# Kernel tuning notes

Hardware: AMD Instinct MI355X
Metric: run time of the kernel (lower is better)

Reference implementation:

```python
import jax, jax.numpy as jnp
import numpy as np

B, N, IN_DIM, HID, OUT_DIM = 8, 1024, 768, 128, 768
H1, H2, MHA_HEADS, C = 8, 1, 4, 32
ALPHA = 0.2
NEG = -9e15
LN_EPS = 1e-5


def _gat_layer(x, W, a1, a2, adj_mask):
    # x: [B,N,Fin], W: [H,Fin,Fout], a1/a2: [H,Fout], adj_mask: [B,N,N] bool
    h = jnp.einsum('bni,hio->bhno', x, W)                      # [B,H,N,F]
    s1 = jnp.einsum('bhno,ho->bhn', h, a1)                     # score for source node i
    s2 = jnp.einsum('bhno,ho->bhn', h, a2)                     # score for target node j
    e = jax.nn.leaky_relu(s1[:, :, :, None] + s2[:, :, None, :], negative_slope=ALPHA)
    e = jnp.where(adj_mask[:, None, :, :], e, NEG)
    attn = jax.nn.softmax(e, axis=-1)                          # [B,H,N,N]
    hp = jnp.einsum('bhnm,bhmo->bhno', attn, h)                # [B,H,N,F]
    b, nh, n, f = hp.shape
    return hp.transpose(0, 2, 1, 3).reshape(b, n, nh * f)      # concat heads -> [B,N,H*F]


def _mha(q, k, v, wq, bq, wk, bk, wv, bv, wo, bo, n_heads):
    # torch-style MultiheadAttention (eval, no dropout). q:[B,Lq,E] k,v:[B,Lk,E]
    b, lq, e = q.shape
    lk = k.shape[1]
    hd = e // n_heads
    Q = (q @ wq + bq).reshape(b, lq, n_heads, hd).transpose(0, 2, 1, 3)
    K = (k @ wk + bk).reshape(b, lk, n_heads, hd).transpose(0, 2, 1, 3)
    V = (v @ wv + bv).reshape(b, lk, n_heads, hd).transpose(0, 2, 1, 3)
    scores = jnp.einsum('bhqd,bhkd->bhqk', Q, K) / jnp.sqrt(jnp.float32(hd))
    attn = jax.nn.softmax(scores, axis=-1)
    out = jnp.einsum('bhqk,bhkd->bhqd', attn, V)
    out = out.transpose(0, 2, 1, 3).reshape(b, lq, e)
    return out @ wo + bo


def _layernorm(x, g, b):
    mu = jnp.mean(x, axis=-1, keepdims=True)
    var = jnp.var(x, axis=-1, keepdims=True)
    return (x - mu) * jax.lax.rsqrt(var + LN_EPS) * g + b


def setup_inputs() -> dict:
    key = jax.random.key(0)
    ks = jax.random.split(key, 24)
    s = lambda fan_in: 1.0 / np.sqrt(fan_in)
    inp = {
        'node_features': jax.random.normal(ks[0], (B, N, IN_DIM), jnp.float32),
        'adjacency': jax.random.randint(ks[1], (B, N, N), 0, 2, jnp.int32),
        'context_indices': jax.random.randint(ks[2], (B, C), 0, N, jnp.int32),
        # GAT layer 1: 8 heads, in=768 -> out=128 each
        'W1': jax.random.normal(ks[3], (H1, IN_DIM, HID), jnp.float32) * s(IN_DIM),
        'a1_1': jax.random.normal(ks[4], (H1, HID), jnp.float32) * s(2 * HID),
        'a2_1': jax.random.normal(ks[5], (H1, HID), jnp.float32) * s(2 * HID),
        # GAT layer 2: 1 head, in=1024 -> out=128
        'W2': jax.random.normal(ks[6], (H2, HID * H1, HID), jnp.float32) * s(HID * H1),
        'a1_2': jax.random.normal(ks[7], (H2, HID), jnp.float32) * s(2 * HID),
        'a2_2': jax.random.normal(ks[8], (H2, HID), jnp.float32) * s(2 * HID),
        # query MultiheadAttention (embed_dim=128, 4 heads)
        'wq': jax.random.normal(ks[9], (HID, HID), jnp.float32) * s(HID),
        'bq': jnp.zeros((HID,), jnp.float32),
        'wk': jax.random.normal(ks[10], (HID, HID), jnp.float32) * s(HID),
        'bk': jnp.zeros((HID,), jnp.float32),
        'wv': jax.random.normal(ks[11], (HID, HID), jnp.float32) * s(HID),
        'bv': jnp.zeros((HID,), jnp.float32),
        'wo': jax.random.normal(ks[12], (HID, HID), jnp.float32) * s(HID),
        'bo': jnp.zeros((HID,), jnp.float32),
        # projection MLP
        'p1_w': jax.random.normal(ks[13], (HID, HID), jnp.float32) * s(HID),
        'p1_b': jnp.zeros((HID,), jnp.float32),
        'ln_g': jnp.ones((HID,), jnp.float32),
        'ln_b': jnp.zeros((HID,), jnp.float32),
        'p2_w': jax.random.normal(ks[14], (HID, OUT_DIM), jnp.float32) * s(HID),
        'p2_b': jnp.zeros((OUT_DIM,), jnp.float32),
    }
    return inp


def reference(node_features, adjacency, context_indices,
              W1, a1_1, a2_1, W2, a1_2, a2_2,
              wq, bq, wk, bk, wv, bv, wo, bo,
              p1_w, p1_b, ln_g, ln_b, p2_w, p2_b):
    adj_mask = adjacency > 0
    h = jax.nn.elu(_gat_layer(node_features, W1, a1_1, a2_1, adj_mask))  # [B,N,1024]
    h = jax.nn.elu(_gat_layer(h, W2, a1_2, a2_2, adj_mask))              # [B,N,128]
    q = h[:, 0:1, :]                                                      # [B,1,E]
    ctx = jnp.take_along_axis(h, context_indices[:, :, None], axis=1)     # [B,C,E]
    pooled = _mha(q, ctx, ctx, wq, bq, wk, bk, wv, bv, wo, bo, MHA_HEADS)[:, 0, :]
    z = jax.nn.relu(_layernorm(pooled @ p1_w + p1_b, ln_g, ln_b))
    return z @ p2_w + p2_b                                                # [B,OUT_DIM]
```

## Files before the change

### kernel.cpp

```cpp
#include <hip/hip_runtime.h>
#include <hip/hip_bf16.h>

#define ALPHA 0.2f
#define LOG2E 1.4426950408889634f

using short8  = __attribute__((ext_vector_type(8))) short;
using short4v = __attribute__((ext_vector_type(4))) short;
using f32x4   = __attribute__((ext_vector_type(4))) float;
using int4v   = __attribute__((ext_vector_type(4))) int;

static __device__ __forceinline__ float b2f(short s) {
    union { float f; unsigned u; } v; v.u = ((unsigned)(unsigned short)s) << 16; return v.f;
}
static __device__ __forceinline__ short f2bf(float f) {
    __hip_bfloat16 h = __float2bfloat16(f);
    return *reinterpret_cast<short*>(&h);
}
static __device__ __forceinline__ float fexp2(float x) {
    return __builtin_amdgcn_exp2f(x);
}
static __device__ __forceinline__ void gload_lds16(const void* g, void* l) {
    __builtin_amdgcn_global_load_lds(
        (const __attribute__((address_space(1))) unsigned*)g,
        (__attribute__((address_space(3))) unsigned*)l, 16, 0, 0);
}

__global__ __launch_bounds__(256) void k_prep(
        const int* __restrict__ adj, unsigned* __restrict__ adjb,
        const float* __restrict__ x, short* __restrict__ xb,
        const float* __restrict__ W1, short* __restrict__ W1T,
        const float* __restrict__ W2, short* __restrict__ W2T) {
    int bid = blockIdx.x, t = threadIdx.x;
    if (bid < 32768) {
        int idx = bid * 256 + t;
        int lane = t & 63;
        unsigned long long m = __ballot(adj[idx] > 0);
        if ((lane & 31) == 0) adjb[idx >> 5] = (unsigned)(m >> (lane & 32));
    } else if (bid < 38912) {
        int idx = (bid - 32768) * 256 + t;
        f32x4 v = ((const f32x4*)x)[idx];
        short4v o;
        o[0] = f2bf(v[0]); o[1] = f2bf(v[1]); o[2] = f2bf(v[2]); o[3] = f2bf(v[3]);
        ((short4v*)xb)[idx] = o;
    } else if (bid < 41984) {
        int idx = (bid - 38912) * 256 + t;
        int n = idx / 768, k = idx - n * 768;
        int h = n >> 7, o = n & 127;
        W1T[idx] = f2bf(W1[(h * 768 + k) * 128 + o]);
    } else {
        int idx = (bid - 41984) * 256 + t;
        int n = idx >> 10, k = idx & 1023;
        W2T[idx] = f2bf(W2[k * 128 + n]);
    }
}

__global__ __launch_bounds__(256) void k_gemm_bt(
        const short* __restrict__ A, const short* __restrict__ Bt,
        short* __restrict__ Ct, int K, int Ncols,
        const float* __restrict__ a1, const float* __restrict__ a2,
        float* __restrict__ s1, float* __restrict__ s2) {
    int tid = threadIdx.x, wave = tid >> 6, lane = tid & 63;
    int lr = lane & 15, lg = lane >> 4;
    int flat = blockIdx.y * gridDim.x + blockIdx.x;
    int chunkw = (gridDim.x * gridDim.y) >> 3;
    int swz = (flat & 7) * chunkw + (flat >> 3);
    int bx = swz % gridDim.x, by = swz / gridDim.x;
    int m0 = bx * 128, n0 = by * 128;
    int wm = (wave >> 1) * 64, wn = (wave & 1) * 64;
    __shared__ short lsA[2][128 * 64], lsB[2][128 * 64];
    __shared__ float sred1[2][128], sred2[2][128];
    f32x4 acc[4][4];
#pragma unroll
    for (int i = 0; i < 4; i++)
#pragma unroll
        for (int j = 0; j < 4; j++) acc[i][j] = (f32x4){0.f, 0.f, 0.f, 0.f};

    auto stage = [&](int bufsel, int k0) {
#pragma unroll
        for (int s = 0; s < 4; s++) {
            int chunk = s * 256 + tid;
            int r = chunk >> 3, c = chunk & 7;
            int csrc = c ^ (r & 7);
            gload_lds16(A + (size_t)(m0 + r) * K + k0 + csrc * 8, &lsA[bufsel][chunk * 8]);
            gload_lds16(Bt + (size_t)(n0 + r) * K + k0 + csrc * 8, &lsB[bufsel][chunk * 8]);
        }
    };
    auto compute = [&](const short* la, const short* lb) {
#pragma unroll
        for (int kk = 0; kk < 2; kk++) {
            short8 a[4], bb[4];
#pragma unroll
            for (int f = 0; f < 4; f++) {
                int ra = wm + f * 16 + lr, rb = wn + f * 16 + lr;
                a[f]  = *(const short8*)(la + ra * 64 + (((kk * 4 + lg) ^ (ra & 7)) * 8));
                bb[f] = *(const short8*)(lb + rb * 64 + (((kk * 4 + lg) ^ (rb & 7)) * 8));
            }
#pragma unroll
            for (int fm = 0; fm < 4; fm++)
#pragma unroll
                for (int fn = 0; fn < 4; fn++)
                    acc[fm][fn] = __builtin_amdgcn_mfma_f32_16x16x32_bf16(a[fm], bb[fn], acc[fm][fn], 0, 0, 0);
        }
    };
    stage(0, 0);
    __syncthreads();
    for (int k2 = 0; k2 < K; k2 += 128) {
        stage(1, k2 + 64);
        compute(lsA[0], lsB[0]);
        __syncthreads();
        if (k2 + 128 < K) stage(0, k2 + 128);
        compute(lsA[1], lsB[1]);
        __syncthreads();
    }
    short* stg = &lsA[0][0];
#pragma unroll
    for (int fm = 0; fm < 4; fm++) {
#pragma unroll
        for (int fn = 0; fn < 4; fn++) {
            int nl = wn + fn * 16 + lr;
            int i4w = (wm + fm * 16 + lg * 4) >> 2;
            short4v st;
            st[0] = f2bf(acc[fm][fn][0]); st[1] = f2bf(acc[fm][fn][1]);
            st[2] = f2bf(acc[fm][fn][2]); st[3] = f2bf(acc[fm][fn][3]);
            *(short4v*)(stg + (nl * 32 + (i4w ^ (nl & 31))) * 4) = st;
        }
    }
    __syncthreads();
    size_t gbase = ((size_t)(m0 >> 10) * Ncols + n0) * 1024 + (m0 & 1023);
#pragma unroll
    for (int it = 0; it < 8; it++) {
        int idx8 = it * 256 + tid;
        int nl = idx8 >> 4, p = idx8 & 15;
        int i4a = 2 * p, i4b = 2 * p + 1;
        short4v lo = *(short4v*)(stg + (nl * 32 + (i4a ^ (nl & 31))) * 4);
        short4v hi = *(short4v*)(stg + (nl * 32 + (i4b ^ (nl & 31))) * 4);
        short8 v;
#pragma unroll
        for (int r = 0; r < 4; r++) { v[r] = lo[r]; v[r + 4] = hi[r]; }
        *(short8*)(Ct + gbase + (size_t)nl * 1024 + p * 8) = v;
    }
    if (a1 != nullptr) {
        int h = by;
        float av1[4], av2[4];
#pragma unroll
        for (int fn = 0; fn < 4; fn++) {
            int o = wn + fn * 16 + lr;
            av1[fn] = a1[h * 128 + o];
            av2[fn] = a2[h * 128 + o];
        }
        int wcol = wave & 1;
#pragma unroll
        for (int fm = 0; fm < 4; fm++)
#pragma unroll
            for (int r = 0; r < 4; r++) {
                float v1 = acc[fm][0][r] * av1[0] + acc[fm][1][r] * av1[1]
                         + acc[fm][2][r] * av1[2] + acc[fm][3][r] * av1[3];
                float v2 = acc[fm][0][r] * av2[0] + acc[fm][1][r] * av2[1]
                         + acc[fm][2][r] * av2[2] + acc[fm][3][r] * av2[3];
#pragma unroll
                for (int off = 1; off < 16; off <<= 1) {
                    v1 += __shfl_xor(v1, off);
                    v2 += __shfl_xor(v2, off);
                }
                if (lr == 0) {
                    int il = wm + fm * 16 + lg * 4 + r;
                    sred1[wcol][il] = v1;
                    sred2[wcol][il] = v2;
                }
            }
        __syncthreads();
        if (tid < 128) {
            int b = m0 >> 10;
            int irow = (b * 8 + h) * 1024 + (m0 & 1023) + tid;
            s1[irow] = (sred1[0][tid] + sred1[1][tid]) * LOG2E;
            s2[irow] = (sred2[0][tid] + sred2[1][tid]) * LOG2E;
        }
    }
}

__global__ __launch_bounds__(256) void k_gemm64(
        const short* __restrict__ A, const short* __restrict__ Bt,
        short* __restrict__ Ct, int K, int Ncols) {
    int tid = threadIdx.x, wave = tid >> 6, lane = tid & 63;
    int lr = lane & 15, lg = lane >> 4;
    int flat = blockIdx.y * gridDim.x + blockIdx.x;
    int chunkw = (gridDim.x * gridDim.y) >> 3;
    int swz = (flat & 7) * chunkw + (flat >> 3);
    int bx = swz % gridDim.x, by = swz / gridDim.x;
    int m0 = bx * 64, n0 = by * 64;
    int wm = (wave >> 1) * 32, wn = (wave & 1) * 32;
    __shared__ short lsA[2][64 * 32], lsB[2][64 * 32];
    f32x4 acc[2][2];
#pragma unroll
    for (int i = 0; i < 2; i++)
#pragma unroll
        for (int j = 0; j < 2; j++) acc[i][j] = (f32x4){0.f, 0.f, 0.f, 0.f};

    auto stage = [&](int bufsel, int k0) {
        int r = tid >> 2, c = tid & 3;
        int csrc = c ^ (r & 3);
        int base = (wave * 64) * 8;
        gload_lds16(A + (size_t)(m0 + r) * K + k0 + csrc * 8, &lsA[bufsel][base]);
        gload_lds16(Bt + (size_t)(n0 + r) * K + k0 + csrc * 8, &lsB[bufsel][base]);
    };
    stage(0, 0);
    __syncthreads();
    int buf = 0;
    for (int k0 = 0; k0 < K; k0 += 32) {
        if (k0 + 32 < K) stage(buf ^ 1, k0 + 32);
        short8 a[2], bb[2];
#pragma unroll
        for (int f = 0; f < 2; f++) {
            int ra = wm + f * 16 + lr, rb = wn + f * 16 + lr;
            a[f]  = *(const short8*)(&lsA[buf][ra * 32 + ((lg ^ (ra & 3)) * 8)]);
            bb[f] = *(const short8*)(&lsB[buf][rb * 32 + ((lg ^ (rb & 3)) * 8)]);
        }
#pragma unroll
        for (int fm = 0; fm < 2; fm++)
#pragma unroll
            for (int fn = 0; fn < 2; fn++)
                acc[fm][fn] = __builtin_amdgcn_mfma_f32_16x16x32_bf16(a[fm], bb[fn], acc[fm][fn], 0, 0, 0);
        __syncthreads();
        buf ^= 1;
    }
#pragma unroll
    for (int fm = 0; fm < 2; fm++) {
        int mb = m0 + wm + fm * 16 + lg * 4;
        size_t obase = ((size_t)(mb >> 10) * Ncols) * 1024 + (mb & 1023);
#pragma unroll
        for (int fn = 0; fn < 2; fn++) {
            int n = n0 + wn + fn * 16 + lr;
            short4v st;
            st[0] = f2bf(acc[fm][fn][0]); st[1] = f2bf(acc[fm][fn][1]);
            st[2] = f2bf(acc[fm][fn][2]); st[3] = f2bf(acc[fm][fn][3]);
            *(short4v*)(Ct + obase + (size_t)n * 1024) = st;
        }
    }
}

__global__ __launch_bounds__(256) void k_s12(
        const short* __restrict__ ht, const float* __restrict__ a1,
        const float* __restrict__ a2, float* __restrict__ s1,
        float* __restrict__ s2, int nh) {
    int bh = blockIdx.x;
    int h = bh % nh;
    int i4 = threadIdx.x * 4;
    const short* base = ht + (size_t)bh * 131072 + i4;
    f32x4 acc1 = {0.f, 0.f, 0.f, 0.f}, acc2 = {0.f, 0.f, 0.f, 0.f};
#pragma unroll 8
    for (int o = 0; o < 128; o++) {
        short4v v = *(const short4v*)(base + ((size_t)o << 10));
        float w1 = a1[h * 128 + o], w2 = a2[h * 128 + o];
#pragma unroll
        for (int r = 0; r < 4; r++) {
            float f = b2f(v[r]);
            acc1[r] += f * w1;
            acc2[r] += f * w2;
        }
    }
#pragma unroll
    for (int r = 0; r < 4; r++) { acc1[r] *= LOG2E; acc2[r] *= LOG2E; }
    *(f32x4*)(s1 + bh * 1024 + i4) = acc1;
    *(f32x4*)(s2 + bh * 1024 + i4) = acc2;
}

__global__ __launch_bounds__(512) void k_attn1(
        const short* __restrict__ ht, const unsigned* __restrict__ adjb,
        const float* __restrict__ s1, const float* __restrict__ s2,
        short* __restrict__ out) {
    int flat = blockIdx.y * 8 + blockIdx.x;
    int swz = (flat & 7) * 64 + (flat >> 3);
    int bh = swz >> 3, bxi = swz & 7;
    int b = bh >> 3, h = bh & 7;
    int tid = threadIdx.x, wave = tid >> 6, lane = tid & 63;
    int lr = lane & 15, lg = lane >> 4;
    int ic = bxi * 128 + wave * 16 + lr;
    int row = bh * 1024 + ic;
    float s1i = s1[row];
    const unsigned long long* abrow =
        (const unsigned long long*)(adjb + ((size_t)(b << 10) + ic) * 32);
    const float* s2r = s2 + bh * 1024;
    const short* hbase = ht + (size_t)bh * 131072;

    __shared__ short lsh[2][16384];
    __shared__ float ls2[1024];
    f32x4 acc[8];
#pragma unroll
    for (int f = 0; f < 8; f++) acc[f] = (f32x4){0.f, 0.f, 0.f, 0.f};
    f32x4 accs = (f32x4){0.f, 0.f, 0.f, 0.f};
    short8 ones8;
#pragma unroll
    for (int e = 0; e < 8; e++) ones8[e] = (short)0x3F80;

    auto stage = [&](int bufsel, int j0) {
#pragma unroll
        for (int s = 0; s < 4; s++) {
            int chunk = s * 512 + tid;
            int r = chunk >> 4, c = chunk & 15;
            int csrc = c ^ (r & 15);
            gload_lds16(hbase + (size_t)r * 1024 + j0 + csrc * 8,
                        &lsh[bufsel][chunk * 8]);
        }
    };
    auto compute = [&](const short* ls, int j0) {
        unsigned long long aw0 = abrow[j0 >> 6], aw1 = abrow[(j0 >> 6) + 1];
#pragma unroll
        for (int kk = 0; kk < 4; kk++) {
            int jb = j0 + kk * 32 + lg * 8;
            f32x4 t0 = *(const f32x4*)(&ls2[jb]);
            f32x4 t1 = *(const f32x4*)(&ls2[jb + 4]);
            unsigned long long aw = (kk < 2) ? aw0 : aw1;
            unsigned bits = (unsigned)(aw >> ((kk & 1) * 32 + lg * 8)) & 0xFFu;
            float pv[8];
#pragma unroll
            for (int e = 0; e < 8; e++) {
                float sv = e < 4 ? t0[e] : t1[e & 3];
                float ee = s1i + sv;
                ee = fmaxf(ee, ALPHA * ee);
                float p = fexp2(ee);
                pv[e] = ((bits >> e) & 1) ? p : 0.f;
            }
            int4v pw;
#pragma unroll
            for (int w = 0; w < 4; w++) {
                int d;
                asm("v_cvt_pk_bf16_f32 %0, %1, %2"
                    : "=v"(d) : "v"(pv[2 * w]), "v"(pv[2 * w + 1]));
                pw[w] = d;
            }
            short8 pb = __builtin_bit_cast(short8, pw);
            __builtin_amdgcn_s_setprio(1);
            accs = __builtin_amdgcn_mfma_f32_16x16x32_bf16(ones8, pb, accs, 0, 0, 0);
#pragma unroll
            for (int fm = 0; fm < 8; fm++) {
                int r = fm * 16 + lr;
                int ck = (kk * 4 + lg) ^ (r & 15);
                short8 af = *(const short8*)(ls + r * 128 + ck * 8);
                acc[fm] = __builtin_amdgcn_mfma_f32_16x16x32_bf16(af, pb, acc[fm], 0, 0, 0);
            }
            __builtin_amdgcn_s_setprio(0);
        }
    };

    if (wave < 4) {
        gload_lds16(s2r + (size_t)(wave * 64 + lane) * 4, &ls2[wave * 256]);
    }
    stage(0, 0);
    __syncthreads();
    for (int t2 = 0; t2 < 1024; t2 += 256) {
        stage(1, t2 + 128);
        compute(lsh[0], t2);
        __syncthreads();
        if (t2 + 256 < 1024) stage(0, t2 + 256);
        compute(lsh[1], t2 + 128);
        __syncthreads();
    }
    float rdi = 1.f / accs[0];
    size_t orow = ((size_t)(b << 10) + ic) * 1024 + h * 128;
#pragma unroll
    for (int fm = 0; fm < 8; fm++) {
        int ob = (fm << 4) + lg * 4;
        short4v st;
#pragma unroll
        for (int r = 0; r < 4; r++) {
            float x = acc[fm][r] * rdi;
            x = x > 0.f ? x : expm1f(x);
            st[r] = f2bf(x);
        }
        *(short4v*)(out + orow + ob) = st;
    }
}

__global__ __launch_bounds__(256) void k_attn2g(
        const short* __restrict__ h2t, const unsigned* __restrict__ adjb,
        const float* __restrict__ s1, const float* __restrict__ s2,
        const int* __restrict__ cidx, float* __restrict__ ghat) {
    int tile = blockIdx.x;
    int b = blockIdx.y;
    int tid = threadIdx.x, wave = tid >> 6, lane = tid & 63;
    int lr = lane & 15, lg = lane >> 4;

    __shared__ int nodes[16];
    __shared__ float sps[4][16];
    __shared__ float sacc[4][16][129];

    if (tid < 16) {
        int pos = tile * 16 + tid;
        int nd = 0;
        if (pos >= 1 && pos <= 32) nd = cidx[b * 32 + pos - 1];
        nodes[tid] = nd;
    }
    __syncthreads();

    const float* s2r = s2 + b * 1024;
    int nd = nodes[lr];
    float s1i = s1[b * 1024 + nd];
    const unsigned long long* abrow =
        (const unsigned long long*)(adjb + ((size_t)(b << 10) + nd) * 32);
    const short* hb = h2t + (size_t)b * 131072;
    f32x4 acc[8];
#pragma unroll
    for (int f = 0; f < 8; f++) acc[f] = (f32x4){0.f, 0.f, 0.f, 0.f};
    float psum = 0.f;

    for (int j0 = wave * 256; j0 < wave * 256 + 256; j0 += 32) {
        int jb = j0 + lg * 8;
        f32x4 t0 = *(const f32x4*)(s2r + jb);
        f32x4 t1 = *(const f32x4*)(s2r + jb + 4);
        unsigned bits = (unsigned)(abrow[j0 >> 6] >> ((j0 & 32) + lg * 8)) & 0xFFu;
        short8 pb;
#pragma unroll
        for (int e = 0; e < 8; e++) {
            float sv = e < 4 ? t0[e] : t1[e & 3];
            float ee = s1i + sv;
            ee = fmaxf(ee, ALPHA * ee);
            float p = fexp2(ee);
            p = ((bits >> e) & 1) ? p : 0.f;
            psum += p;
            pb[e] = f2bf(p);
        }
#pragma unroll
        for (int fm = 0; fm < 8; fm++) {
            short8 af = *(const short8*)(hb + (size_t)(fm * 16 + lr) * 1024 + jb);
            acc[fm] = __builtin_amdgcn_mfma_f32_16x16x32_bf16(af, pb, acc[fm], 0, 0, 0);
        }
    }
    psum += __shfl_xor(psum, 16);
    psum += __shfl_xor(psum, 32);
    if (lg == 0) sps[wave][lr] = psum;
#pragma unroll
    for (int fm = 0; fm < 8; fm++)
#pragma unroll
        for (int r = 0; r < 4; r++)
            sacc[wave][lr][fm * 16 + lg * 4 + r] = acc[fm][r];
    __syncthreads();
    for (int e = tid; e < 2048; e += 256) {
        int li = e >> 7, o = e & 127;
        float sum = sps[0][li] + sps[1][li] + sps[2][li] + sps[3][li];
        float v = (sacc[0][li][o] + sacc[1][li][o] + sacc[2][li][o] + sacc[3][li][o]) / sum;
        v = v > 0.f ? v : expm1f(v);
        ghat[((size_t)b * 48 + tile * 16 + li) * 128 + o] = v;
    }
}

__global__ __launch_bounds__(256) void k_qkv(
        const float* __restrict__ ghat,
        const float* __restrict__ wk, const float* __restrict__ bk,
        const float* __restrict__ wvp, const float* __restrict__ bv,
        float* __restrict__ Kp, float* __restrict__ Vp) {
    int b = blockIdx.y, rg = blockIdx.x & 7, o0 = (blockIdx.x >> 3) * 64;
    int t = threadIdx.x, wvi = t >> 6, ln = t & 63;
    __shared__ float sx[4][128];
    __shared__ float sWk[128 * 64], sWv[128 * 64];

    if (wvi < 2) {
        int cb = wvi * 64;
        gload_lds16(ghat + ((size_t)b * 48 + 1 + rg * 4) * 128 + (size_t)(cb + ln) * 4,
                    (float*)sx + cb * 4);
    }
#pragma unroll
    for (int s = 0; s < 8; s++) {
        int cb = s * 256 + wvi * 64;
        int q = cb + ln, rw = q >> 4, c4 = q & 15;
        gload_lds16(wk  + (size_t)rw * 128 + o0 + c4 * 4, &sWk[cb * 4]);
        gload_lds16(wvp + (size_t)rw * 128 + o0 + c4 * 4, &sWv[cb * 4]);
    }
    __syncthreads();
    int o = o0 + ln;
    float ka = bk[o], va = bv[o];
#pragma unroll 32
    for (int c = 0; c < 128; c++) {
        float x = sx[wvi][c];
        ka += x * sWk[c * 64 + ln];
        va += x * sWv[c * 64 + ln];
    }
    int r = rg * 4 + wvi;
    Kp[((size_t)b * 32 + r) * 128 + o] = ka;
    Vp[((size_t)b * 32 + r) * 128 + o] = va;
}

__global__ __launch_bounds__(256) void k_tail(
        const float* __restrict__ ghat, const float* __restrict__ Kp,
        const float* __restrict__ Vp,
        const float* __restrict__ wq, const float* __restrict__ bq,
        const float* __restrict__ wo, const float* __restrict__ bo,
        const float* __restrict__ p1w, const float* __restrict__ p1b,
        const float* __restrict__ lng, const float* __restrict__ lnb,
        float* __restrict__ tvec) {
    int b = blockIdx.x, t = threadIdx.x;
    int wvi = t >> 6, ln = t & 63;
    __shared__ float sq[128], sQ[128], sK[32][128], sV[32][128];
    __shared__ float sP[4][33], sO[128], sT[128], sZ[128];
    __shared__ float sred[2];
    __shared__ float sW[128 * 128];

#pragma unroll
    for (int s = 0; s < 4; s++) {
        int cb = s * 256 + wvi * 64;
        gload_lds16(Kp + (size_t)b * 4096 + (size_t)(cb + ln) * 4, (float*)sK + cb * 4);
        gload_lds16(Vp + (size_t)b * 4096 + (size_t)(cb + ln) * 4, (float*)sV + cb * 4);
    }
#pragma unroll
    for (int s = 0; s < 16; s++) {
        int cb = s * 256 + wvi * 64;
        gload_lds16(wq + (size_t)(cb + ln) * 4, &sW[cb * 4]);
    }
    if (t < 128) sq[t] = ghat[(size_t)b * 48 * 128 + t];
    __syncthreads();
    if (t < 128) {
        float a0 = 0.f, a1 = 0.f, a2 = 0.f, a3 = 0.f;
#pragma unroll
        for (int c = 0; c < 128; c += 4) {
            a0 += sq[c]     * sW[c * 128 + t];
            a1 += sq[c + 1] * sW[(c + 1) * 128 + t];
            a2 += sq[c + 2] * sW[(c + 2) * 128 + t];
            a3 += sq[c + 3] * sW[(c + 3) * 128 + t];
        }
        sQ[t] = bq[t] + ((a0 + a1) + (a2 + a3));
    }
    __syncthreads();
#pragma unroll
    for (int s = 0; s < 16; s++) {
        int cb = s * 256 + wvi * 64;
        gload_lds16(wo + (size_t)(cb + ln) * 4, &sW[cb * 4]);
    }
    if (t < 128) {
        int hh = t >> 5, jj = t & 31;
        float s = 0.f;
#pragma unroll
        for (int d = 0; d < 32; d++) s += sQ[hh * 32 + d] * sK[jj][hh * 32 + d];
        s *= 0.17677669529663687f;
        float m = s;
#pragma unroll
        for (int off = 16; off > 0; off >>= 1) m = fmaxf(m, __shfl_xor(m, off, 32));
        float p = __expf(s - m);
        float sum = p;
#pragma unroll
        for (int off = 16; off > 0; off >>= 1) sum += __shfl_xor(sum, off, 32);
        sP[hh][jj] = p / sum;
    }
    __syncthreads();
    if (t < 128) {
        int hh = t >> 5;
        float s = 0.f;
#pragma unroll
        for (int jj = 0; jj < 32; jj++) s += sP[hh][jj] * sV[jj][t];
        sO[t] = s;
    }
    __syncthreads();
    if (t < 128) {
        float a0 = 0.f, a1 = 0.f, a2 = 0.f, a3 = 0.f;
#pragma unroll
        for (int c = 0; c < 128; c += 4) {
            a0 += sO[c]     * sW[c * 128 + t];
            a1 += sO[c + 1] * sW[(c + 1) * 128 + t];
            a2 += sO[c + 2] * sW[(c + 2) * 128 + t];
            a3 += sO[c + 3] * sW[(c + 3) * 128 + t];
        }
        sT[t] = bo[t] + ((a0 + a1) + (a2 + a3));
    }
    __syncthreads();
#pragma unroll
    for (int s = 0; s < 16; s++) {
        int cb = s * 256 + wvi * 64;
        gload_lds16(p1w + (size_t)(cb + ln) * 4, &sW[cb * 4]);
    }
    __syncthreads();
    if (t < 128) {
        float a0 = 0.f, a1 = 0.f, a2 = 0.f, a3 = 0.f;
#pragma unroll
        for (int c = 0; c < 128; c += 4) {
            a0 += sT[c]     * sW[c * 128 + t];
            a1 += sT[c + 1] * sW[(c + 1) * 128 + t];
            a2 += sT[c + 2] * sW[(c + 2) * 128 + t];
            a3 += sT[c + 3] * sW[(c + 3) * 128 + t];
        }
        sZ[t] = p1b[t] + ((a0 + a1) + (a2 + a3));
    }
    __syncthreads();
    if (t < 64) {
        float v = sZ[t] + sZ[t + 64];
#pragma unroll
        for (int off = 32; off > 0; off >>= 1) v += __shfl_xor(v, off);
        if (t == 0) sred[0] = v * (1.f / 128.f);
    }
    __syncthreads();
    float mu = sred[0];
    if (t < 64) {
        float d1 = sZ[t] - mu, d2 = sZ[t + 64] - mu;
        float v = d1 * d1 + d2 * d2;
#pragma unroll
        for (int off = 32; off > 0; off >>= 1) v += __shfl_xor(v, off);
        if (t == 0) sred[1] = v * (1.f / 128.f);
    }
    __syncthreads();
    float rstd = rsqrtf(sred[1] + 1e-5f);
    if (t < 128) {
        float z = (sZ[t] - mu) * rstd * lng[t] + lnb[t];
        tvec[b * 128 + t] = fmaxf(z, 0.f);
    }
}

__global__ __launch_bounds__(256) void k_p2(
        const float* __restrict__ tvec, const float* __restrict__ p2w,
        const float* __restrict__ p2b, float* __restrict__ out) {
    int jj0 = blockIdx.x * 128, b = blockIdx.y;
    int t = threadIdx.x, wvi = t >> 6, ln = t & 63;
    __shared__ float sT[128];
    __shared__ float sW[128 * 128];

#pragma unroll
    for (int s = 0; s < 16; s++) {
        int cb = s * 256 + wvi * 64;
        int q = cb + ln, c = q >> 5, c4 = q & 31;
        gload_lds16(p2w + (size_t)c * 768 + jj0 + c4 * 4, &sW[cb * 4]);
    }
    if (t < 128) sT[t] = tvec[b * 128 + t];
    __syncthreads();
    if (t < 128) {
        float a0 = 0.f, a1 = 0.f, a2 = 0.f, a3 = 0.f;
#pragma unroll
        for (int c = 0; c < 128; c += 4) {
            a0 += sT[c]     * sW[c * 128 + t];
            a1 += sT[c + 1] * sW[(c + 1) * 128 + t];
            a2 += sT[c + 2] * sW[(c + 2) * 128 + t];
            a3 += sT[c + 3] * sW[(c + 3) * 128 + t];
        }
        out[b * 768 + jj0 + t] = p2b[jj0 + t] + ((a0 + a1) + (a2 + a3));
    }
}

extern "C" void kernel_launch(void* const* d_in, const int* in_sizes, int n_in,
                              void* d_out, int out_size, void* d_ws, size_t ws_size,
                              hipStream_t stream) {
    const float* x   = (const float*)d_in[0];
    const int*  adj  = (const int*)d_in[1];
    const int*  cidx = (const int*)d_in[2];
    const float* W1  = (const float*)d_in[3];
    const float* a11 = (const float*)d_in[4];
    const float* a21 = (const float*)d_in[5];
    const float* W2  = (const float*)d_in[6];
    const float* a12 = (const float*)d_in[7];
    const float* a22 = (const float*)d_in[8];
    const float* wq = (const float*)d_in[9];  const float* bq = (const float*)d_in[10];
    const float* wk = (const float*)d_in[11]; const float* bk = (const float*)d_in[12];
    const float* wv = (const float*)d_in[13]; const float* bv = (const float*)d_in[14];
    const float* wo = (const float*)d_in[15]; const float* bo = (const float*)d_in[16];
    const float* p1w = (const float*)d_in[17]; const float* p1b = (const float*)d_in[18];
    const float* lng = (const float*)d_in[19]; const float* lnb = (const float*)d_in[20];
    const float* p2w = (const float*)d_in[21]; const float* p2b = (const float*)d_in[22];
    float* out = (float*)d_out;

    char* ws = (char*)d_ws;
    size_t off = 0;
    auto alloc = [&](size_t bytes) -> char* {
        char* p = ws + off;
        off = (off + bytes + 255) & ~(size_t)255;
        return p;
    };
    short* Xb   = (short*)alloc(8192ull * 768 * 2);
    short* W1T  = (short*)alloc(1024ull * 768 * 2);
    short* W2T  = (short*)alloc(128ull * 1024 * 2);
    unsigned* adjb = (unsigned*)alloc(8ull * 1024 * 32 * 4);
    short* h1t  = (short*)alloc(64ull * 128 * 1024 * 2);
    float* s1a  = (float*)alloc(64ull * 1024 * 4);
    float* s2a  = (float*)alloc(64ull * 1024 * 4);
    short* hcat = (short*)alloc(8192ull * 1024 * 2);
    short* h2t  = (short*)alloc(8ull * 128 * 1024 * 2);
    float* s1b  = (float*)alloc(8192ull * 4);
    float* s2b  = (float*)alloc(8192ull * 4);
    float* ghat = (float*)alloc(8ull * 48 * 128 * 4);
    float* Kp   = (float*)alloc(8ull * 32 * 128 * 4);
    float* Vp   = (float*)alloc(8ull * 32 * 128 * 4);
    float* tvec = (float*)alloc(8ull * 128 * 4);
    if (off > ws_size) return;

    k_prep<<<42496, 256, 0, stream>>>(adj, adjb, x, Xb, W1, W1T, W2, W2T);

    k_gemm_bt<<<dim3(64, 8), 256, 0, stream>>>(Xb, W1T, h1t, 768, 1024,
                                               a11, a21, s1a, s2a);
    k_attn1<<<dim3(8, 64), 512, 0, stream>>>(h1t, adjb, s1a, s2a, hcat);

    k_gemm64<<<dim3(128, 2), 256, 0, stream>>>(hcat, W2T, h2t, 1024, 128);
    k_s12<<<8, 256, 0, stream>>>(h2t, a12, a22, s1b, s2b, 1);
    k_attn2g<<<dim3(3, 8), 256, 0, stream>>>(h2t, adjb, s1b, s2b, cidx, ghat);

    k_qkv<<<dim3(16, 8), 256, 0, stream>>>(ghat, wk, bk, wv, bv, Kp, Vp);
    k_tail<<<8, 256, 0, stream>>>(ghat, Kp, Vp, wq, bq, wo, bo,
                                  p1w, p1b, lng, lnb, tvec);
    k_p2<<<dim3(6, 8), 256, 0, stream>>>(tvec, p2w, p2b, out);
}
```

Measured before the change: 148.4 us.

## Fuse second-layer GAT score computation into attention kernel, drop setprio

Removes the separate k_s12 launch and computes the layer-2 attention scores inside k_attn2g. Each block computes the s2 scores for all 1024 nodes into LDS and s1 only for its 16 query nodes. This saves one kernel launch and the global round-trip for the score arrays. The cost is that each of the 24 blocks recomputes the full s2 vector, repeating the work three times per batch. It also drops the s_setprio bracketing around the MFMA section of k_attn1, which may change wave scheduling there.

```diff
diff --git a/kernel.cpp b/kernel.cpp
--- a/kernel.cpp
+++ b/kernel.cpp
@@ -238,32 +238,6 @@
     }
 }
 
-__global__ __launch_bounds__(256) void k_s12(
-        const short* __restrict__ ht, const float* __restrict__ a1,
-        const float* __restrict__ a2, float* __restrict__ s1,
-        float* __restrict__ s2, int nh) {
-    int bh = blockIdx.x;
-    int h = bh % nh;
-    int i4 = threadIdx.x * 4;
-    const short* base = ht + (size_t)bh * 131072 + i4;
-    f32x4 acc1 = {0.f, 0.f, 0.f, 0.f}, acc2 = {0.f, 0.f, 0.f, 0.f};
-#pragma unroll 8
-    for (int o = 0; o < 128; o++) {
-        short4v v = *(const short4v*)(base + ((size_t)o << 10));
-        float w1 = a1[h * 128 + o], w2 = a2[h * 128 + o];
-#pragma unroll
-        for (int r = 0; r < 4; r++) {
-            float f = b2f(v[r]);
-            acc1[r] += f * w1;
-            acc2[r] += f * w2;
-        }
-    }
-#pragma unroll
-    for (int r = 0; r < 4; r++) { acc1[r] *= LOG2E; acc2[r] *= LOG2E; }
-    *(f32x4*)(s1 + bh * 1024 + i4) = acc1;
-    *(f32x4*)(s2 + bh * 1024 + i4) = acc2;
-}
-
 __global__ __launch_bounds__(512) void k_attn1(
         const short* __restrict__ ht, const unsigned* __restrict__ adjb,
         const float* __restrict__ s1, const float* __restrict__ s2,
@@ -329,7 +303,6 @@
                 pw[w] = d;
             }
             short8 pb = __builtin_bit_cast(short8, pw);
-            __builtin_amdgcn_s_setprio(1);
             accs = __builtin_amdgcn_mfma_f32_16x16x32_bf16(ones8, pb, accs, 0, 0, 0);
 #pragma unroll
             for (int fm = 0; fm < 8; fm++) {
@@ -338,7 +311,6 @@
                 short8 af = *(const short8*)(ls + r * 128 + ck * 8);
                 acc[fm] = __builtin_amdgcn_mfma_f32_16x16x32_bf16(af, pb, acc[fm], 0, 0, 0);
             }
-            __builtin_amdgcn_s_setprio(0);
         }
     };
 
@@ -373,7 +345,7 @@
 
 __global__ __launch_bounds__(256) void k_attn2g(
         const short* __restrict__ h2t, const unsigned* __restrict__ adjb,
-        const float* __restrict__ s1, const float* __restrict__ s2,
+        const float* __restrict__ a1, const float* __restrict__ a2,
         const int* __restrict__ cidx, float* __restrict__ ghat) {
     int tile = blockIdx.x;
     int b = blockIdx.y;
@@ -381,23 +353,60 @@
     int lr = lane & 15, lg = lane >> 4;
 
     __shared__ int nodes[16];
+    __shared__ float ss1[16];
+    __shared__ float sp1[16][17];
+    __shared__ float ls2q[1024];
     __shared__ float sps[4][16];
     __shared__ float sacc[4][16][129];
 
+    const short* hb = h2t + (size_t)b * 131072;
+
     if (tid < 16) {
         int pos = tile * 16 + tid;
-        int nd = 0;
-        if (pos >= 1 && pos <= 32) nd = cidx[b * 32 + pos - 1];
-        nodes[tid] = nd;
-    }
-    __syncthreads();
-
-    const float* s2r = s2 + b * 1024;
+        int nd0 = 0;
+        if (pos >= 1 && pos <= 32) nd0 = cidx[b * 32 + pos - 1];
+        nodes[tid] = nd0;
+    }
+    {
+        int j4 = wave * 256 + lane * 4;
+        const short* base = hb + j4;
+        f32x4 a2v = {0.f, 0.f, 0.f, 0.f};
+#pragma unroll 8
+        for (int o = 0; o < 128; o++) {
+            short4v v = *(const short4v*)(base + ((size_t)o << 10));
+            float w2 = a2[o];
+#pragma unroll
+            for (int r = 0; r < 4; r++) a2v[r] += b2f(v[r]) * w2;
+        }
+#pragma unroll
+        for (int r = 0; r < 4; r++) a2v[r] *= LOG2E;
+        *(f32x4*)(&ls2q[j4]) = a2v;
+    }
+    __syncthreads();
+    {
+        int nd1 = nodes[tid & 15];
+        int oc = tid >> 4;
+        float p1 = 0.f;
+#pragma unroll
+        for (int oo = 0; oo < 8; oo++) {
+            int o = oc * 8 + oo;
+            p1 += b2f(hb[((size_t)o << 10) + nd1]) * a1[o];
+        }
+        sp1[oc][tid & 15] = p1;
+    }
+    __syncthreads();
+    if (tid < 16) {
+        float s = 0.f;
+#pragma unroll
+        for (int oc = 0; oc < 16; oc++) s += sp1[oc][tid];
+        ss1[tid] = s * LOG2E;
+    }
+    __syncthreads();
+
     int nd = nodes[lr];
-    float s1i = s1[b * 1024 + nd];
+    float s1i = ss1[lr];
     const unsigned long long* abrow =
         (const unsigned long long*)(adjb + ((size_t)(b << 10) + nd) * 32);
-    const short* hb = h2t + (size_t)b * 131072;
     f32x4 acc[8];
 #pragma unroll
     for (int f = 0; f < 8; f++) acc[f] = (f32x4){0.f, 0.f, 0.f, 0.f};
@@ -405,8 +414,8 @@
 
     for (int j0 = wave * 256; j0 < wave * 256 + 256; j0 += 32) {
         int jb = j0 + lg * 8;
-        f32x4 t0 = *(const f32x4*)(s2r + jb);
-        f32x4 t1 = *(const f32x4*)(s2r + jb + 4);
+        f32x4 t0 = *(const f32x4*)(&ls2q[jb]);
+        f32x4 t1 = *(const f32x4*)(&ls2q[jb + 4]);
         unsigned bits = (unsigned)(abrow[j0 >> 6] >> ((j0 & 32) + lg * 8)) & 0xFFu;
         short8 pb;
 #pragma unroll
@@ -667,8 +676,6 @@
     float* s2a  = (float*)alloc(64ull * 1024 * 4);
     short* hcat = (short*)alloc(8192ull * 1024 * 2);
     short* h2t  = (short*)alloc(8ull * 128 * 1024 * 2);
-    float* s1b  = (float*)alloc(8192ull * 4);
-    float* s2b  = (float*)alloc(8192ull * 4);
     float* ghat = (float*)alloc(8ull * 48 * 128 * 4);
     float* Kp   = (float*)alloc(8ull * 32 * 128 * 4);
     float* Vp   = (float*)alloc(8ull * 32 * 128 * 4);
@@ -682,8 +689,7 @@
     k_attn1<<<dim3(8, 64), 512, 0, stream>>>(h1t, adjb, s1a, s2a, hcat);
 
     k_gemm64<<<dim3(128, 2), 256, 0, stream>>>(hcat, W2T, h2t, 1024, 128);
-    k_s12<<<8, 256, 0, stream>>>(h2t, a12, a22, s1b, s2b, 1);
-    k_attn2g<<<dim3(3, 8), 256, 0, stream>>>(h2t, adjb, s1b, s2b, cidx, ghat);
+    k_attn2g<<<dim3(3, 8), 256, 0, stream>>>(h2t, adjb, a12, a22, cidx, ghat);
 
     k_qkv<<<dim3(16, 8), 256, 0, stream>>>(ghat, wk, bk, wv, bv, Kp, Vp);
     k_tail<<<8, 256, 0, stream>>>(ghat, Kp, Vp, wq, bq, wo, bo,
```

After: 136.5 us (median of 2 runs). 1.09x faster.
